# Kernel tuning notes

Hardware: AMD Instinct MI355X
Metric: run time of the kernel (lower is better)

The kernel has to match this reference:

```python
import jax, jax.numpy as jnp
import numpy as np

B, S, D, H, DH = 2, 2048, 1024, 16, 64
ATTN_SCALE = float(np.sqrt(DH))  # use_attn_scale=True -> sqrt(d_head)
IGNORE = -100000.0


def setup_inputs() -> dict:
    key = jax.random.key(0)
    ks = jax.random.split(key, 8)
    init = 0.02
    return {
        "residual": jax.random.normal(ks[0], (B, S, D), dtype=jnp.float32),
        "x": jax.random.normal(ks[1], (B, S, D), dtype=jnp.float32),
        "W_Q": jax.random.normal(ks[2], (H, D, DH), dtype=jnp.float32) * init,
        "W_K": jax.random.normal(ks[3], (H, D, DH), dtype=jnp.float32) * init,
        "W_V": jax.random.normal(ks[4], (H, D, DH), dtype=jnp.float32) * init,
        "W_O": jax.random.normal(ks[5], (H, DH, D), dtype=jnp.float32) * init,
        "b_Q": jnp.zeros((H, DH), dtype=jnp.float32),
        "b_K": jnp.zeros((H, DH), dtype=jnp.float32),
        "b_V": jnp.zeros((H, DH), dtype=jnp.float32),
        "b_O": jnp.zeros((D,), dtype=jnp.float32),
    }


def reference(residual, x, W_Q, W_K, W_V, W_O, b_Q, b_K, b_V, b_O):
    # QKV projections: [b,s,d] x [h,d,e] -> [b,s,h,e]
    q = jnp.einsum("bsd,hde->bshe", x, W_Q) + b_Q
    k = jnp.einsum("bsd,hde->bshe", x, W_K) + b_K
    v = jnp.einsum("bsd,hde->bshe", x, W_V) + b_V
    # Scores: [b,h,q,k]
    attn_scores = jnp.einsum("bqhe,bkhe->bhqk", q, k) / ATTN_SCALE
    causal = jnp.tril(jnp.ones((S, S), dtype=bool))
    attn_scores = jnp.where(causal, attn_scores, IGNORE)
    pattern = jax.nn.softmax(attn_scores, axis=-1)
    # Weighted values: [b,q,h,e]
    z = jnp.einsum("bkhe,bhqk->bqhe", v, pattern)
    out = jnp.einsum("bqhe,hed->bqd", z, W_O) + b_O
    return (residual, out)
```

## Files before the change

kernel.cpp:

```cpp
#include <hip/hip_runtime.h>
#include <hip/hip_bf16.h>

#define BB 2
#define SS 2048
#define DD 1024
#define HH 16
#define DHD 64

typedef __attribute__((ext_vector_type(8))) short short8;
typedef __attribute__((ext_vector_type(4))) float floatx4;
typedef __attribute__((ext_vector_type(16))) float floatx16;
typedef __attribute__((ext_vector_type(4))) unsigned short ushortx4;

static __device__ __forceinline__ unsigned short f2bf(float f) {
    union { __hip_bfloat16 h; unsigned short u; } cv;
    cv.h = __float2bfloat16(f);
    return cv.u;
}

typedef __attribute__((address_space(1))) const unsigned int* gas_t;
typedef __attribute__((address_space(3))) unsigned int* las_t;
static __device__ __forceinline__ void g2l16(const void* g, void* l) {
    __builtin_amdgcn_global_load_lds((gas_t)g, (las_t)l, 16, 0, 0);
}

#define SW(row, c8) ((c8) ^ ((row) & 7))

static __device__ __forceinline__ unsigned cvt_pk_bf16(float lo, float hi) {
    unsigned r;
    asm("v_cvt_pk_bf16_f32 %0, %1, %2" : "=v"(r) : "v"(lo), "v"(hi));
    return r;
}
static __device__ __forceinline__ void pl32_swap(unsigned &a, unsigned &b) {
    asm("v_permlane32_swap_b32 %0, %1" : "+v"(a), "+v"(b));
}

__global__ __launch_bounds__(256) void prep(const float4* __restrict__ residual4,
        float4* __restrict__ out4,
        const float* __restrict__ x, unsigned short* __restrict__ xb,
        const float* __restrict__ WQ, const float* __restrict__ WK,
        const float* __restrict__ WV, unsigned short* __restrict__ Wt,
        const float* __restrict__ WO, unsigned short* __restrict__ WtO) {
    __shared__ float tile[64][65];
    const int bid = blockIdx.x;
    const int t = threadIdx.x;

    if (bid < 1024) {
        size_t base = (size_t)bid * 1024 + t;
#pragma unroll
        for (int j = 0; j < 4; j++) out4[base + j * 256] = residual4[base + j * 256];
    } else if (bid < 3072) {
        size_t i = ((size_t)(bid - 1024) * 256 + t) * 8;
        const float4* src4 = (const float4*)(x + i);
        float4 a = src4[0], b = src4[1];
        short8 o;
        o[0] = (short)f2bf(a.x); o[1] = (short)f2bf(a.y);
        o[2] = (short)f2bf(a.z); o[3] = (short)f2bf(a.w);
        o[4] = (short)f2bf(b.x); o[5] = (short)f2bf(b.y);
        o[6] = (short)f2bf(b.z); o[7] = (short)f2bf(b.w);
        *(short8*)(xb + i) = o;
    } else if (bid < 3840) {
        int u = bid - 3072;
        const int d0 = (u & 15) * 64;
        const int h  = (u >> 4) & 15;
        const int which = u >> 8;
        const float* W = (which == 0) ? WQ : (which == 1) ? WK : WV;
        const float* src = W + (size_t)h * DD * DHD;
#pragma unroll
        for (int i = 0; i < 16; i++) {
            int idx = i * 256 + t;
            int r = idx >> 6, c = idx & 63;
            tile[r][c] = src[(size_t)(d0 + r) * DHD + c];
        }
        __syncthreads();
        unsigned short* dst = Wt + ((size_t)which * 1024 + h * 64) * DD;
#pragma unroll
        for (int i = 0; i < 16; i++) {
            int idx = i * 256 + t;
            int e = idx >> 6, d = idx & 63;
            dst[(size_t)e * DD + d0 + d] = f2bf(tile[d][e]);
        }
    } else {
        int u = bid - 3840;
        const int k0 = (u & 15) * 64;
        const int n0 = (u >> 4) * 64;
#pragma unroll
        for (int i = 0; i < 16; i++) {
            int idx = i * 256 + t;
            int r = idx >> 6, c = idx & 63;
            tile[r][c] = WO[(size_t)(k0 + r) * DD + n0 + c];
        }
        __syncthreads();
#pragma unroll
        for (int i = 0; i < 16; i++) {
            int idx = i * 256 + t;
            int n = idx >> 6, kk = idx & 63;
            WtO[(size_t)(n0 + n) * DD + k0 + kk] = f2bf(tile[kk][n]);
        }
    }
}

__global__ __launch_bounds__(256) void qkv_mfma(const unsigned short* __restrict__ xb,
        const unsigned short* __restrict__ Wt,
        const float* __restrict__ bQ, const float* __restrict__ bK,
        const float* __restrict__ bV,
        unsigned short* __restrict__ oq, unsigned short* __restrict__ ok,
        unsigned short* __restrict__ ov) {
    __shared__ unsigned short smem[32768];

    const int m0 = blockIdx.x * 128;
    const int y  = blockIdx.y;
    const int which = y >> 3;
    const int h0 = (y & 7) * 2;
    const float* bias = (which == 0) ? bQ : (which == 1) ? bK : bV;
    unsigned short* ob = (which == 0) ? oq : (which == 1) ? ok : ov;
    const float scale = (which == 0) ? 0.18033688f : 1.0f;
    const unsigned short* Wb = Wt + (size_t)y * 128 * DD;

    const int t = threadIdx.x;
    const int lane = t & 63, w = t >> 6;
    const int l15 = lane & 15, quad = lane >> 4;

    floatx4 acc[2][8];
#pragma unroll
    for (int mt = 0; mt < 2; mt++)
#pragma unroll
        for (int nt = 0; nt < 8; nt++) acc[mt][nt] = floatx4{0.f, 0.f, 0.f, 0.f};

#pragma unroll
    for (int i = 0; i < 4; i++) {
        int c = i * 256 + t;
        int row = c >> 3, c8 = c & 7;
        g2l16(xb + (size_t)(m0 + row) * DD + SW(row, c8) * 8, smem + c * 8);
        g2l16(Wb + (size_t)row * DD + SW(row, c8) * 8, smem + 16384 + c * 8);
    }

    int buf = 0;
    for (int k0 = 0; k0 < DD; k0 += 64) {
        __syncthreads();
        if (k0 + 64 < DD) {
            const int nb = buf ^ 1;
#pragma unroll
            for (int i = 0; i < 4; i++) {
                int c = i * 256 + t;
                int row = c >> 3, c8 = c & 7;
                g2l16(xb + (size_t)(m0 + row) * DD + k0 + 64 + SW(row, c8) * 8,
                      smem + nb * 8192 + c * 8);
                g2l16(Wb + (size_t)row * DD + k0 + 64 + SW(row, c8) * 8,
                      smem + 16384 + nb * 8192 + c * 8);
            }
        }
        const unsigned short* As = smem + buf * 8192;
        const unsigned short* Bs = smem + 16384 + buf * 8192;
#pragma unroll
        for (int ks = 0; ks < 2; ks++) {
            short8 af[2], bf[8];
#pragma unroll
            for (int mt = 0; mt < 2; mt++)
                af[mt] = *(const short8*)(As + (w * 32 + mt * 16 + l15) * 64 +
                                          SW(l15, ks * 4 + quad) * 8);
#pragma unroll
            for (int nt = 0; nt < 8; nt++)
                bf[nt] = *(const short8*)(Bs + (nt * 16 + l15) * 64 +
                                          SW(l15, ks * 4 + quad) * 8);
#pragma unroll
            for (int mt = 0; mt < 2; mt++)
#pragma unroll
                for (int nt = 0; nt < 8; nt++)
                    acc[mt][nt] = __builtin_amdgcn_mfma_f32_16x16x32_bf16(
                        af[mt], bf[nt], acc[mt][nt], 0, 0, 0);
        }
        buf ^= 1;
    }
    __syncthreads();

    if (which == 2) {
        unsigned short* T = smem;
#pragma unroll
        for (int mt = 0; mt < 2; mt++)
#pragma unroll
            for (int r = 0; r < 4; r++) {
                int mloc = w * 32 + mt * 16 + quad * 4 + r;
#pragma unroll
                for (int nt = 0; nt < 8; nt++) {
                    int n = nt * 16 + l15;
                    int h = h0 + (n >> 6), e = n & 63;
                    T[n * 132 + mloc] = f2bf(acc[mt][nt][r] + bias[h * DHD + e]);
                }
            }
        __syncthreads();
        const int b = m0 >> 11;
        const int s_base = m0 & (SS - 1);
#pragma unroll
        for (int i = 0; i < 8; i++) {
            int u = i * 256 + t;
            int row = u >> 4, c8 = u & 15;
            int h = h0 + (row >> 6), e = row & 63;
            *(short8*)(ov + (((size_t)b * HH + h) * DHD + e) * SS + s_base + c8 * 8) =
                *(const short8*)(T + row * 132 + c8 * 8);
        }
    } else {
#pragma unroll
        for (int mt = 0; mt < 2; mt++) {
#pragma unroll
            for (int r = 0; r < 4; r++) {
                int m = m0 + w * 32 + mt * 16 + quad * 4 + r;
                int b = m >> 11, s = m & (SS - 1);
#pragma unroll
                for (int nt = 0; nt < 8; nt++) {
                    int h = h0 + (nt >> 2);
                    int e = (nt & 3) * 16 + l15;
                    float v = (acc[mt][nt][r] + bias[h * DHD + e]) * scale;
                    ob[(((size_t)b * HH + h) * SS + s) * DHD + e] = f2bf(v);
                }
            }
        }
    }
}

#define KVT 128
__global__ __launch_bounds__(512, 4) void attn(const unsigned short* __restrict__ q,
        const unsigned short* __restrict__ k, const unsigned short* __restrict__ vt,
        unsigned short* __restrict__ z) {
    __shared__ unsigned short smem[32768];

    const int i0 = blockIdx.x;
    int bh, qt;
    if (i0 < 256) { bh = i0 & 31;         qt = 15 - (i0 >> 5); }
    else          { bh = (i0 - 256) & 31; qt = (i0 - 256) >> 5; }
    const int b  = bh >> 4, h = bh & (HH - 1);
    const int q0 = qt * 128;

    const int t = threadIdx.x;
    const int lane = t & 63;
    const int w = t >> 6;
    const int qsub = w & 3;
    const int grp  = w >> 2;
    const int l31 = lane & 31;
    const int hi = lane >> 5;

    const unsigned short* qb  = q  + (size_t)bh * SS * DHD;
    const unsigned short* kb  = k  + (size_t)bh * SS * DHD;
    const unsigned short* vtb = vt + (size_t)bh * DHD * SS;

    const int qrow = q0 + qsub * 32 + l31;
    const int fmin = q0 + qsub * 32;

    short8 qf[4];
#pragma unroll
    for (int c = 0; c < 4; c++)
        qf[c] = *(const short8*)(qb + (size_t)qrow * DHD + c * 16 + hi * 8);

    floatx16 o_acc[2];
#pragma unroll
    for (int eh = 0; eh < 2; eh++)
#pragma unroll
        for (int i = 0; i < 16; i++) o_acc[eh][i] = 0.f;
    float lsum = 0.f;

    int koff[4], voff[4];
#pragma unroll
    for (int c = 0; c < 4; c++)
        koff[c] = (grp * 64 + l31) * 64 + (((2 * c + hi) ^ (l31 & 7)) * 8);
#pragma unroll
    for (int ch = 0; ch < 4; ch++)
        voff[ch] = l31 * 128 + (((grp * 8 + ch * 2 + hi) ^ (l31 & 15)) * 8);

    const int nit = qt + 1;

#pragma unroll
    for (int i = 0; i < 2; i++) {
        int u = i * 512 + t, r = u >> 3, c8 = u & 7;
        g2l16(kb + (size_t)r * DHD + (c8 ^ (r & 7)) * 8, smem + u * 8);
    }
#pragma unroll
    for (int i = 0; i < 2; i++) {
        int u = i * 512 + t, e = u >> 4, c16 = u & 15;
        g2l16(vtb + (size_t)e * SS + (c16 ^ (e & 15)) * 8, smem + 16384 + u * 8);
    }

    for (int it = 0; it < nit; it++) {
        const int cur = it & 1;
        __syncthreads();
        if (it + 1 < nit) {
            const int nxt = cur ^ 1;
            const int kbase = (it + 1) * KVT;
#pragma unroll
            for (int i = 0; i < 2; i++) {
                int u = i * 512 + t, r = u >> 3, c8 = u & 7;
                g2l16(kb + (size_t)(kbase + r) * DHD + (c8 ^ (r & 7)) * 8,
                      smem + nxt * 8192 + u * 8);
            }
#pragma unroll
            for (int i = 0; i < 2; i++) {
                int u = i * 512 + t, e = u >> 4, c16 = u & 15;
                g2l16(vtb + (size_t)e * SS + kbase + (c16 ^ (e & 15)) * 8,
                      smem + 16384 + nxt * 8192 + u * 8);
            }
        }

        const unsigned short* Kc = smem + cur * 8192;
        const unsigned short* Vc = smem + 16384 + cur * 8192;
        const int tb = it * KVT + grp * 64;

#pragma unroll
        for (int st = 0; st < 2; st++) {
            const int kvb = tb + st * 32;
            if (kvb > fmin + 31) continue;

            floatx16 sacc;
#pragma unroll
            for (int i = 0; i < 16; i++) sacc[i] = 0.f;
            __builtin_amdgcn_s_setprio(1);
#pragma unroll
            for (int c = 0; c < 4; c++) {
                short8 af = *(const short8*)(Kc + st * 2048 + koff[c]);
                sacc = __builtin_amdgcn_mfma_f32_32x32x16_bf16(af, qf[c], sacc,
                                                               0, 0, 0);
            }
            __builtin_amdgcn_s_setprio(0);

            unsigned wv[8];
            if (kvb + 31 <= fmin) {
#pragma unroll
                for (int r2 = 0; r2 < 8; r2++) {
                    float p0 = __builtin_amdgcn_exp2f(sacc[2 * r2]);
                    float p1 = __builtin_amdgcn_exp2f(sacc[2 * r2 + 1]);
                    lsum += p0 + p1;
                    wv[r2] = cvt_pk_bf16(p0, p1);
                }
            } else {
#pragma unroll
                for (int r2 = 0; r2 < 8; r2++) {
                    const int ra = 2 * r2, rb = 2 * r2 + 1;
                    const int kva = kvb + (ra & 3) + 8 * (ra >> 2) + 4 * hi;
                    const int kvc = kvb + (rb & 3) + 8 * (rb >> 2) + 4 * hi;
                    float p0 = (kva <= qrow) ? __builtin_amdgcn_exp2f(sacc[ra]) : 0.f;
                    float p1 = (kvc <= qrow) ? __builtin_amdgcn_exp2f(sacc[rb]) : 0.f;
                    lsum += p0 + p1;
                    wv[r2] = cvt_pk_bf16(p0, p1);
                }
            }
            pl32_swap(wv[0], wv[2]);
            pl32_swap(wv[1], wv[3]);
            pl32_swap(wv[4], wv[6]);
            pl32_swap(wv[5], wv[7]);
            union { unsigned u[4]; short8 s; } u0, u1;
            u0.u[0] = wv[0]; u0.u[1] = wv[1]; u0.u[2] = wv[2]; u0.u[3] = wv[3];
            u1.u[0] = wv[4]; u1.u[1] = wv[5]; u1.u[2] = wv[6]; u1.u[3] = wv[7];
            const short8 pb0 = u0.s, pb1 = u1.s;

            __builtin_amdgcn_s_setprio(1);
#pragma unroll
            for (int eh = 0; eh < 2; eh++) {
                short8 vf0 = *(const short8*)(Vc + eh * 4096 + voff[2 * st]);
                o_acc[eh] = __builtin_amdgcn_mfma_f32_32x32x16_bf16(
                    vf0, pb0, o_acc[eh], 0, 0, 0);
                short8 vf1 = *(const short8*)(Vc + eh * 4096 + voff[2 * st + 1]);
                o_acc[eh] = __builtin_amdgcn_mfma_f32_32x32x16_bf16(
                    vf1, pb1, o_acc[eh], 0, 0, 0);
            }
            __builtin_amdgcn_s_setprio(0);
        }
    }

    lsum += __shfl_xor(lsum, 32);
    float* cm = (float*)smem;
    float* slot = cm + (qsub * 64 + lane) * 33;
    __syncthreads();
    if (grp == 1) {
#pragma unroll
        for (int eh = 0; eh < 2; eh++)
#pragma unroll
            for (int i = 0; i < 16; i++) slot[eh * 16 + i] = o_acc[eh][i];
        slot[32] = lsum;
    }
    __syncthreads();
    if (grp == 0) {
#pragma unroll
        for (int eh = 0; eh < 2; eh++)
#pragma unroll
            for (int i = 0; i < 16; i++) o_acc[eh][i] += slot[eh * 16 + i];
        const float inv = 1.f / (lsum + slot[32]);
        unsigned short* zr = z + ((size_t)b * SS + qrow) * (HH * DHD) + h * DHD;
#pragma unroll
        for (int eh = 0; eh < 2; eh++)
#pragma unroll
            for (int g = 0; g < 4; g++) {
                ushortx4 o;
#pragma unroll
                for (int m = 0; m < 4; m++) o[m] = f2bf(o_acc[eh][g * 4 + m] * inv);
                *(ushortx4*)(zr + eh * 32 + g * 8 + 4 * hi) = o;
            }
    }
}

__global__ __launch_bounds__(256) void out_mfma(const unsigned short* __restrict__ zb,
        const unsigned short* __restrict__ WtO, const float* __restrict__ bo,
        float* __restrict__ out) {
    __shared__ unsigned short smem[16384];

    const int m0 = blockIdx.x * 64;
    const int n0 = blockIdx.y * 64;
    const int t = threadIdx.x;
    const int lane = t & 63, w = t >> 6;
    const int l15 = lane & 15, quad = lane >> 4;

    floatx4 acc[4];
#pragma unroll
    for (int nt = 0; nt < 4; nt++) acc[nt] = floatx4{0.f, 0.f, 0.f, 0.f};

#pragma unroll
    for (int i = 0; i < 2; i++) {
        int c = i * 256 + t;
        int row = c >> 3, c8 = c & 7;
        g2l16(zb + (size_t)(m0 + row) * DD + SW(row, c8) * 8, smem + c * 8);
        g2l16(WtO + (size_t)(n0 + row) * DD + SW(row, c8) * 8, smem + 8192 + c * 8);
    }

    int buf = 0;
    for (int k0 = 0; k0 < DD; k0 += 64) {
        __syncthreads();
        if (k0 + 64 < DD) {
            const int nb = buf ^ 1;
#pragma unroll
            for (int i = 0; i < 2; i++) {
                int c = i * 256 + t;
                int row = c >> 3, c8 = c & 7;
                g2l16(zb + (size_t)(m0 + row) * DD + k0 + 64 + SW(row, c8) * 8,
                      smem + nb * 4096 + c * 8);
                g2l16(WtO + (size_t)(n0 + row) * DD + k0 + 64 + SW(row, c8) * 8,
                      smem + 8192 + nb * 4096 + c * 8);
            }
        }
        const unsigned short* As = smem + buf * 4096;
        const unsigned short* Bs = smem + 8192 + buf * 4096;
#pragma unroll
        for (int ks = 0; ks < 2; ks++) {
            short8 af = *(const short8*)(As + (w * 16 + l15) * 64 +
                                         SW(l15, ks * 4 + quad) * 8);
#pragma unroll
            for (int nt = 0; nt < 4; nt++) {
                short8 bf = *(const short8*)(Bs + (nt * 16 + l15) * 64 +
                                             SW(l15, ks * 4 + quad) * 8);
                acc[nt] = __builtin_amdgcn_mfma_f32_16x16x32_bf16(
                    af, bf, acc[nt], 0, 0, 0);
            }
        }
        buf ^= 1;
    }
#pragma unroll
    for (int r = 0; r < 4; r++) {
        int m = m0 + w * 16 + quad * 4 + r;
#pragma unroll
        for (int nt = 0; nt < 4; nt++) {
            int n = n0 + nt * 16 + l15;
            out[(size_t)m * DD + n] = acc[nt][r] + bo[n];
        }
    }
}

extern "C" void kernel_launch(void* const* d_in, const int* in_sizes, int n_in,
                              void* d_out, int out_size, void* d_ws, size_t ws_size,
                              hipStream_t stream) {
    const float* residual = (const float*)d_in[0];
    const float* x   = (const float*)d_in[1];
    const float* W_Q = (const float*)d_in[2];
    const float* W_K = (const float*)d_in[3];
    const float* W_V = (const float*)d_in[4];
    const float* W_O = (const float*)d_in[5];
    const float* b_Q = (const float*)d_in[6];
    const float* b_K = (const float*)d_in[7];
    const float* b_V = (const float*)d_in[8];
    const float* b_O = (const float*)d_in[9];
    float* out = (float*)d_out;

    const size_t NE = (size_t)BB * SS * HH * DHD;
    unsigned short* xb  = (unsigned short*)d_ws;
    unsigned short* Wt  = xb + (size_t)4096 * 1024;
    unsigned short* WtO = Wt + (size_t)3072 * 1024;
    unsigned short* qb  = WtO + (size_t)1024 * 1024;
    unsigned short* kb  = qb + NE;
    unsigned short* vb  = kb + NE;
    unsigned short* zb  = vb + NE;

    prep<<<4096, 256, 0, stream>>>((const float4*)residual, (float4*)out,
                                   x, xb, W_Q, W_K, W_V, Wt, W_O, WtO);

    qkv_mfma<<<dim3(32, 24), 256, 0, stream>>>(xb, Wt, b_Q, b_K, b_V, qb, kb, vb);

    attn<<<512, 512, 0, stream>>>(qb, kb, vb, zb);

    out_mfma<<<dim3(64, 16), 256, 0, stream>>>(
        zb, WtO, b_O, out + (size_t)BB * SS * DD);
}
```

Baseline: 176.0 us.

## Batch PV MFMAs after both score subtiles and enlarge out-projection M tile

In the attention kernel, both 32-wide score subtiles are now computed and converted to bf16 probabilities first, and the PV MFMAs for all four chunks are issued together afterwards. This lets score MFMAs and exp work from the second subtile overlap with the first, at the cost of keeping more probability registers live. The output projection GEMM tile grows from 64 to 128 rows per block, with each wave computing two M subtiles. That reuses every loaded W_O fragment twice and halves the grid, but raises LDS and register use.

```diff
diff --git a/kernel.cpp b/kernel.cpp
--- a/kernel.cpp
+++ b/kernel.cpp
@@ -302,11 +302,16 @@
         const unsigned short* Kc = smem + cur * 8192;
         const unsigned short* Vc = smem + 16384 + cur * 8192;
         const int tb = it * KVT + grp * 64;
+        const bool alive0 = (tb      <= fmin + 31);
+        const bool alive1 = (tb + 32 <= fmin + 31);
+
+        short8 pb[4];
 
 #pragma unroll
         for (int st = 0; st < 2; st++) {
+            const bool alive = st ? alive1 : alive0;
+            if (!alive) continue;
             const int kvb = tb + st * 32;
-            if (kvb > fmin + 31) continue;
 
             floatx16 sacc;
 #pragma unroll
@@ -348,20 +353,22 @@
             union { unsigned u[4]; short8 s; } u0, u1;
             u0.u[0] = wv[0]; u0.u[1] = wv[1]; u0.u[2] = wv[2]; u0.u[3] = wv[3];
             u1.u[0] = wv[4]; u1.u[1] = wv[5]; u1.u[2] = wv[6]; u1.u[3] = wv[7];
-            const short8 pb0 = u0.s, pb1 = u1.s;
-
-            __builtin_amdgcn_s_setprio(1);
+            pb[2 * st]     = u0.s;
+            pb[2 * st + 1] = u1.s;
+        }
+
+        __builtin_amdgcn_s_setprio(1);
+#pragma unroll
+        for (int ch = 0; ch < 4; ch++) {
+            if (!((ch >> 1) ? alive1 : alive0)) continue;
 #pragma unroll
             for (int eh = 0; eh < 2; eh++) {
-                short8 vf0 = *(const short8*)(Vc + eh * 4096 + voff[2 * st]);
+                short8 vf = *(const short8*)(Vc + eh * 4096 + voff[ch]);
                 o_acc[eh] = __builtin_amdgcn_mfma_f32_32x32x16_bf16(
-                    vf0, pb0, o_acc[eh], 0, 0, 0);
-                short8 vf1 = *(const short8*)(Vc + eh * 4096 + voff[2 * st + 1]);
-                o_acc[eh] = __builtin_amdgcn_mfma_f32_32x32x16_bf16(
-                    vf1, pb1, o_acc[eh], 0, 0, 0);
-            }
-            __builtin_amdgcn_s_setprio(0);
-        }
+                    vf, pb[ch], o_acc[eh], 0, 0, 0);
+            }
+        }
+        __builtin_amdgcn_s_setprio(0);
     }
 
     lsum += __shfl_xor(lsum, 32);
@@ -398,24 +405,31 @@
 __global__ __launch_bounds__(256) void out_mfma(const unsigned short* __restrict__ zb,
         const unsigned short* __restrict__ WtO, const float* __restrict__ bo,
         float* __restrict__ out) {
-    __shared__ unsigned short smem[16384];
-
-    const int m0 = blockIdx.x * 64;
+    __shared__ unsigned short smem[24576];
+
+    const int m0 = blockIdx.x * 128;
     const int n0 = blockIdx.y * 64;
     const int t = threadIdx.x;
     const int lane = t & 63, w = t >> 6;
     const int l15 = lane & 15, quad = lane >> 4;
 
-    floatx4 acc[4];
-#pragma unroll
-    for (int nt = 0; nt < 4; nt++) acc[nt] = floatx4{0.f, 0.f, 0.f, 0.f};
-
+    floatx4 acc[2][4];
+#pragma unroll
+    for (int mt = 0; mt < 2; mt++)
+#pragma unroll
+        for (int nt = 0; nt < 4; nt++) acc[mt][nt] = floatx4{0.f, 0.f, 0.f, 0.f};
+
+#pragma unroll
+    for (int i = 0; i < 4; i++) {
+        int c = i * 256 + t;
+        int row = c >> 3, c8 = c & 7;
+        g2l16(zb + (size_t)(m0 + row) * DD + SW(row, c8) * 8, smem + c * 8);
+    }
 #pragma unroll
     for (int i = 0; i < 2; i++) {
         int c = i * 256 + t;
         int row = c >> 3, c8 = c & 7;
-        g2l16(zb + (size_t)(m0 + row) * DD + SW(row, c8) * 8, smem + c * 8);
-        g2l16(WtO + (size_t)(n0 + row) * DD + SW(row, c8) * 8, smem + 8192 + c * 8);
+        g2l16(WtO + (size_t)(n0 + row) * DD + SW(row, c8) * 8, smem + 16384 + c * 8);
     }
 
     int buf = 0;
@@ -424,38 +438,52 @@
         if (k0 + 64 < DD) {
             const int nb = buf ^ 1;
 #pragma unroll
+            for (int i = 0; i < 4; i++) {
+                int c = i * 256 + t;
+                int row = c >> 3, c8 = c & 7;
+                g2l16(zb + (size_t)(m0 + row) * DD + k0 + 64 + SW(row, c8) * 8,
+                      smem + nb * 8192 + c * 8);
+            }
+#pragma unroll
             for (int i = 0; i < 2; i++) {
                 int c = i * 256 + t;
                 int row = c >> 3, c8 = c & 7;
-                g2l16(zb + (size_t)(m0 + row) * DD + k0 + 64 + SW(row, c8) * 8,
-                      smem + nb * 4096 + c * 8);
                 g2l16(WtO + (size_t)(n0 + row) * DD + k0 + 64 + SW(row, c8) * 8,
-                      smem + 8192 + nb * 4096 + c * 8);
-            }
-        }
-        const unsigned short* As = smem + buf * 4096;
-        const unsigned short* Bs = smem + 8192 + buf * 4096;
+                      smem + 16384 + nb * 4096 + c * 8);
+            }
+        }
+        const unsigned short* As = smem + buf * 8192;
+        const unsigned short* Bs = smem + 16384 + buf * 4096;
 #pragma unroll
         for (int ks = 0; ks < 2; ks++) {
-            short8 af = *(const short8*)(As + (w * 16 + l15) * 64 +
-                                         SW(l15, ks * 4 + quad) * 8);
+            short8 af[2], bf[4];
+#pragma unroll
+            for (int mt = 0; mt < 2; mt++)
+                af[mt] = *(const short8*)(As + (w * 32 + mt * 16 + l15) * 64 +
+                                          SW(l15, ks * 4 + quad) * 8);
+#pragma unroll
+            for (int nt = 0; nt < 4; nt++)
+                bf[nt] = *(const short8*)(Bs + (nt * 16 + l15) * 64 +
+                                          SW(l15, ks * 4 + quad) * 8);
+#pragma unroll
+            for (int mt = 0; mt < 2; mt++)
+#pragma unroll
+                for (int nt = 0; nt < 4; nt++)
+                    acc[mt][nt] = __builtin_amdgcn_mfma_f32_16x16x32_bf16(
+                        af[mt], bf[nt], acc[mt][nt], 0, 0, 0);
+        }
+        buf ^= 1;
+    }
+#pragma unroll
+    for (int mt = 0; mt < 2; mt++) {
+#pragma unroll
+        for (int r = 0; r < 4; r++) {
+            int m = m0 + w * 32 + mt * 16 + quad * 4 + r;
 #pragma unroll
             for (int nt = 0; nt < 4; nt++) {
-                short8 bf = *(const short8*)(Bs + (nt * 16 + l15) * 64 +
-                                             SW(l15, ks * 4 + quad) * 8);
-                acc[nt] = __builtin_amdgcn_mfma_f32_16x16x32_bf16(
-                    af, bf, acc[nt], 0, 0, 0);
-            }
-        }
-        buf ^= 1;
-    }
-#pragma unroll
-    for (int r = 0; r < 4; r++) {
-        int m = m0 + w * 16 + quad * 4 + r;
-#pragma unroll
-        for (int nt = 0; nt < 4; nt++) {
-            int n = n0 + nt * 16 + l15;
-            out[(size_t)m * DD + n] = acc[nt][r] + bo[n];
+                int n = n0 + nt * 16 + l15;
+                out[(size_t)m * DD + n] = acc[mt][nt][r] + bo[n];
+            }
         }
     }
 }
@@ -491,6 +519,6 @@
 
     attn<<<512, 512, 0, stream>>>(qb, kb, vb, zb);
 
-    out_mfma<<<dim3(64, 16), 256, 0, stream>>>(
+    out_mfma<<<dim3(32, 16), 256, 0, stream>>>(
         zb, WtO, b_O, out + (size_t)BB * SS * DD);
 }
```

Measured after the change: 179.9 us. 1.02x slower.
